# Kernel optimization log

Measured on AMD Instinct MI355X. Metric: run time of the kernel, lower is better.

Reference implementation:

```python
import jax, jax.numpy as jnp
import numpy as np

N, T, I, H = 32, 2048, 256, 512


def setup_inputs() -> dict:
    key = jax.random.key(0)
    k1, k2, k3, k4, k5 = jax.random.split(key, 5)
    x = jax.random.normal(k1, (N, T, I), dtype=jnp.float32)
    initial = jax.random.normal(k2, (N, H), dtype=jnp.float32)
    # nn.Linear default init: U(-1/sqrt(fan_in), 1/sqrt(fan_in))
    s_ih = 1.0 / np.sqrt(I)
    s_hh = 1.0 / np.sqrt(H)
    W_ih = jax.random.uniform(k3, (H, I), jnp.float32, -s_ih, s_ih)
    b_ih = jax.random.uniform(k4, (H,), jnp.float32, -s_ih, s_ih)
    W_hh = jax.random.uniform(k5, (H, H), jnp.float32, -s_hh, s_hh)
    return {"x": x, "initial": initial, "W_ih": W_ih, "b_ih": b_ih, "W_hh": W_hh}


def reference(x, initial, W_ih, b_ih, W_hh):
    # Precompute input projections for all timesteps: [N, T, H]
    proj = jnp.einsum('nti,hi->nth', x, W_ih) + b_ih
    # h_0 = initial + W_ih x_0 + b
    h0 = initial + proj[:, 0]
    # h_t = W_hh h_{t-1} + W_ih x_{t-1} + b  (note: x index is t-1, faithful to source)
    xs = jnp.swapaxes(proj[:, :-1], 0, 1)  # time-major [T-1, N, H], entries t=0..T-2

    def step(h_prev, p):
        h_new = h_prev @ W_hh.T + p
        return h_new, h_new

    _, hs = jax.lax.scan(step, h0, xs)  # [T-1, N, H]
    hiddens = jnp.concatenate([h0[:, None], jnp.swapaxes(hs, 0, 1)], axis=1)  # [N, T, H]
    return (hiddens, hiddens)
```

## Files before the change

kernel.cpp:

```cpp
#include <hip/hip_runtime.h>

#define NB 32
#define TT 2048
#define II 256
#define HH 512
#define LCH 8
#define NCH 256

typedef short s8v __attribute__((ext_vector_type(8)));
typedef short s4v __attribute__((ext_vector_type(4)));
typedef __bf16 bf8v __attribute__((ext_vector_type(8)));
typedef float f4v __attribute__((ext_vector_type(4)));

#define DEVI static __device__ __forceinline__

DEVI float bf2f(short s){ union{unsigned u; float f;} c; c.u = ((unsigned)(unsigned short)s) << 16; return c.f; }
DEVI short f2bf(float f){ union{float f; unsigned u;} c; c.f = f; unsigned u = c.u; u += 0x7FFF + ((u >> 16) & 1); return (short)(u >> 16); }
DEVI f4v fzero(){ f4v z = {0.0f,0.0f,0.0f,0.0f}; return z; }

DEVI f4v mfma16(s8v a, s8v b, f4v c){
  union{ s8v s; bf8v b; } ua, ub; ua.s = a; ub.s = b;
  return __builtin_amdgcn_mfma_f32_16x16x32_bf16(ua.b, ub.b, c, 0, 0, 0);
}

DEVI s8v ldfrag_bf(const short* base, int row0, int ld, int k0, int lane){
  const short* p = base + (size_t)(row0 + (lane & 15)) * ld + k0 + ((lane >> 4) << 3);
  return *(const s8v*)p;
}
DEVI s8v ldfrag_f32(const float* base, int row0, int ld, int k0, int lane){
  const float* p = base + (size_t)(row0 + (lane & 15)) * ld + k0 + ((lane >> 4) << 3);
  f4v lo = *(const f4v*)p;
  f4v hi = *(const f4v*)(p + 4);
  s8v o;
  o[0]=f2bf(lo[0]); o[1]=f2bf(lo[1]); o[2]=f2bf(lo[2]); o[3]=f2bf(lo[3]);
  o[4]=f2bf(hi[0]); o[5]=f2bf(hi[1]); o[6]=f2bf(hi[2]); o[7]=f2bf(hi[3]);
  return o;
}

DEVI int swzoff(int row, int col){ return (row << 9) + ((((col >> 3) ^ (row & 7)) << 3) | (col & 7)); }

#define RAWBAR() asm volatile("s_waitcnt lgkmcnt(0)\n\ts_barrier" ::: "memory")

DEVI void gload16(const void* g, void* l){
  __builtin_amdgcn_global_load_lds((const __attribute__((address_space(1))) void*)g,
                                   (__attribute__((address_space(3))) void*)l, 16, 0, 0);
}

DEVI void stageB(const short* Bt, int ld, int k0, short* btile, int wave, int lane){
  #pragma unroll
  for(int r = 0; r < 8; ++r){
    int slotbase = (((r << 3) + wave) << 6);
    int slot = slotbase + lane;
    int col = slot >> 3, g = slot & 7;
    int gsrc = g ^ (col & 7);
    gload16(Bt + (size_t)col * ld + k0 + (gsrc << 3), btile + ((size_t)slotbase << 3));
  }
}

DEVI s8v ldB(const short* btile, int col, int q, int kk){
  int gphys = ((kk >> 3) + q) ^ (col & 7);
  return *(const s8v*)(btile + (col << 6) + (gphys << 3));
}

__global__ __launch_bounds__(256) void k_init_p1(const float* __restrict__ W,
                                                 short* __restrict__ mats, short* __restrict__ matsT){
  __shared__ short tile[64][65];
  int bx = blockIdx.x, by = blockIdx.y;
  int t = threadIdx.x;
  for(int i = 0; i < 16; ++i){
    int idx = t + 256*i;
    int rr = idx >> 6, cc = idx & 63;
    short v = f2bf(W[(size_t)(64*by + rr)*HH + 64*bx + cc]);
    tile[rr][cc] = v;
    mats[(size_t)(64*by + rr)*HH + 64*bx + cc] = v;
  }
  __syncthreads();
  for(int i = 0; i < 16; ++i){
    int idx = t + 256*i;
    int rr = idx >> 6, cc = idx & 63;
    matsT[(size_t)(64*bx + rr)*HH + 64*by + cc] = tile[cc][rr];
  }
}

__global__ __launch_bounds__(256) void k_cvt(const float* __restrict__ src, short* __restrict__ dst, int n){
  for(int i = blockIdx.x*256 + threadIdx.x; i < n; i += gridDim.x*256) dst[i] = f2bf(src[i]);
}

struct ProdArgs {
  const short* A[8]; const short* Bt[8]; short* C[8]; short* Ct[8];
};
__global__ __launch_bounds__(256) void k_prod(ProdArgs args){
  int bz = blockIdx.z;
  const short* A  = args.A[bz];
  const short* Bt = args.Bt[bz];
  short* C  = args.C[bz];
  short* Ct = args.Ct[bz];
  int wave = threadIdx.x >> 6, lane = threadIdx.x & 63;
  int mrow0 = blockIdx.x*64 + (wave & 1)*32;
  int ncol0 = blockIdx.y*128 + (wave >> 1)*64;
  f4v acc[2][4];
  for(int mi=0;mi<2;mi++) for(int j=0;j<4;j++) acc[mi][j] = fzero();
  for(int k0 = 0; k0 < HH; k0 += 32){
    s8v a0 = ldfrag_bf(A, mrow0,      HH, k0, lane);
    s8v a1 = ldfrag_bf(A, mrow0 + 16, HH, k0, lane);
    #pragma unroll
    for(int j = 0; j < 4; ++j){
      s8v b = ldfrag_bf(Bt, ncol0 + (j<<4), HH, k0, lane);
      acc[0][j] = mfma16(a0, b, acc[0][j]);
      acc[1][j] = mfma16(a1, b, acc[1][j]);
    }
  }
  int q = lane >> 4, c0 = lane & 15;
  for(int mi=0;mi<2;mi++) for(int j=0;j<4;j++) for(int r=0;r<4;r++){
    int row = mrow0 + (mi<<4) + (q<<2) + r;
    int col = ncol0 + (j<<4) + c0;
    short v = f2bf(acc[mi][j][r]);
    C [(size_t)row*HH + col] = v;
    Ct[(size_t)col*HH + row] = v;
  }
}

__global__ __launch_bounds__(512, 4) void k_proj(const float* __restrict__ x, const short* __restrict__ Wb,
                                                 const float* __restrict__ bih, const float* __restrict__ initial,
                                                 short* __restrict__ projb, float* __restrict__ Y00){
  __shared__ __align__(16) short btile[HH*64];
  int b = blockIdx.x;
  int tid = threadIdx.x, wave = tid >> 6, lane = tid & 63;
  int q = lane >> 4, c0 = lane & 15;
  int ncol0 = wave << 6;
  int mrow0 = b << 5;
  f4v acc[2][4];
  #pragma unroll
  for(int mi=0;mi<2;mi++)
  #pragma unroll
  for(int j=0;j<4;j++) acc[mi][j] = fzero();
  s8v a[2][2], an[2][2];
  #pragma unroll
  for(int mi=0;mi<2;++mi)
  #pragma unroll
  for(int k2=0;k2<2;++k2) a[mi][k2] = ldfrag_f32(x, mrow0 + (mi<<4), II, (k2<<5), lane);
  for(int kc = 0; kc < 4; ++kc){
    stageB(Wb, II, kc << 6, btile, wave, lane);
    if(kc < 3){
      #pragma unroll
      for(int mi=0;mi<2;++mi)
      #pragma unroll
      for(int k2=0;k2<2;++k2) an[mi][k2] = ldfrag_f32(x, mrow0 + (mi<<4), II, ((kc+1)<<6)+(k2<<5), lane);
    }
    __syncthreads();
    #pragma unroll
    for(int k2 = 0; k2 < 2; ++k2){
      int kk = k2 << 5;
      #pragma unroll
      for(int j = 0; j < 4; ++j){
        s8v bb = ldB(btile, ncol0 + (j<<4) + c0, q, kk);
        acc[0][j] = mfma16(a[0][k2], bb, acc[0][j]);
        acc[1][j] = mfma16(a[1][k2], bb, acc[1][j]);
      }
    }
    RAWBAR();
    #pragma unroll
    for(int mi=0;mi<2;++mi)
    #pragma unroll
    for(int k2=0;k2<2;++k2) a[mi][k2] = an[mi][k2];
  }
  short* pstage = btile;
  #pragma unroll
  for(int mi=0;mi<2;++mi)
  #pragma unroll
  for(int j=0;j<4;++j)
  #pragma unroll
  for(int r=0;r<4;++r){
    int rown = (mi<<4) + (q<<2) + r;
    int col  = ncol0 + (j<<4) + c0;
    float v = acc[mi][j][r] + bih[col];
    pstage[rown*HH + col] = f2bf(v);
    if(((b & 63) | rown) == 0){
      int n = mrow0 >> 11;
      Y00[(size_t)n*HH + col] = v + initial[(size_t)n*HH + col];
    }
  }
  RAWBAR();
  #pragma unroll
  for(int rr = 0; rr < 4; ++rr){
    int si = tid + (rr << 9);
    int rn = si >> 6, u = (si & 63) << 3;
    *(s8v*)(projb + ((size_t)(mrow0 + rn))*HH + u) = *(const s8v*)(pstage + rn*HH + u);
  }
}

template<int PHASE>
__global__ __launch_bounds__(512, 2) void k_scan(const short* __restrict__ projb,
                                                 const short* __restrict__ Wb,
                                                 const float* __restrict__ Zin,
                                                 float* __restrict__ Yout){
  __shared__ __align__(16) short btile[HH*64];
  __shared__ __align__(16) short st[NB*HH];
  __shared__ __align__(16) short pbuf[NB*HH];
  int c = blockIdx.x;
  int tid = threadIdx.x, wave = tid >> 6, lane = tid & 63;
  int q = lane >> 4, c0 = lane & 15;
  int ncol0 = wave << 6;
  float* fstage = (float*)btile;
  if(PHASE == 0){
    for(int i = tid; i < NB*HH; i += 512) st[i] = 0;
  } else {
    const float* Z = Zin + (size_t)c*NB*HH;
    #pragma unroll
    for(int rr = 0; rr < 8; ++rr){
      int fi = tid + (rr << 9);
      int rn = fi >> 7, col = (fi & 127) << 2;
      f4v v = *(const f4v*)(Z + (size_t)rn*HH + col);
      s4v sv; sv[0]=f2bf(v[0]); sv[1]=f2bf(v[1]); sv[2]=f2bf(v[2]); sv[3]=f2bf(v[3]);
      *(s4v*)(st + swzoff(rn, col)) = sv;
      if(c == 0) *(f4v*)(Yout + ((size_t)rn*TT)*HH + col) = v;
    }
  }
  RAWBAR();
  int tmax = min(LCH, TT - 1 - LCH*c);
  for(int tl = 1; tl <= tmax; ++tl){
    int t = LCH*c + tl;
    #pragma unroll
    for(int r = 0; r < 4; ++r){
      int rn = wave + (r << 3);
      gload16(projb + ((size_t)rn*TT + (t-1))*HH + ((size_t)lane << 3), pbuf + rn*HH);
    }
    f4v acc[2][4];
    #pragma unroll
    for(int mi=0;mi<2;mi++)
    #pragma unroll
    for(int j=0;j<4;j++) acc[mi][j] = fzero();
    for(int kc = 0; kc < 8; ++kc){
      stageB(Wb, HH, kc << 6, btile, wave, lane);
      __syncthreads();
      #pragma unroll
      for(int k2 = 0; k2 < 2; ++k2){
        int kk = k2 << 5;
        int colb = (kc << 6) + kk + (q << 3);
        s8v a0 = *(const s8v*)(st + swzoff(c0,      colb));
        s8v a1 = *(const s8v*)(st + swzoff(c0 + 16, colb));
        #pragma unroll
        for(int j = 0; j < 4; ++j){
          s8v bb = ldB(btile, ncol0 + (j<<4) + c0, q, kk);
          acc[0][j] = mfma16(a0, bb, acc[0][j]);
          acc[1][j] = mfma16(a1, bb, acc[1][j]);
        }
      }
      RAWBAR();
    }
    #pragma unroll
    for(int mi=0;mi<2;++mi)
    #pragma unroll
    for(int j=0;j<4;++j)
    #pragma unroll
    for(int r=0;r<4;++r){
      int rown = (mi<<4) + (q<<2) + r;
      int col  = ncol0 + (j<<4) + c0;
      float v = acc[mi][j][r] + bf2f(pbuf[rown*HH + col]);
      st[swzoff(rown, col)] = f2bf(v);
      if(PHASE == 0){
        if(tl == LCH && c + 1 < NCH)
          Yout[((size_t)(c+1)*NB + rown)*HH + col] = v;
      } else {
        fstage[rown*HH + col] = v;
      }
    }
    if(PHASE == 1){
      RAWBAR();
      #pragma unroll
      for(int rr = 0; rr < 8; ++rr){
        int fi = tid + (rr << 9);
        int rn = fi >> 7, col = (fi & 127) << 2;
        *(f4v*)(Yout + ((size_t)rn*TT + t)*HH + col) = *(const f4v*)(fstage + (size_t)rn*HH + col);
      }
    }
    RAWBAR();
  }
}

__global__ __launch_bounds__(512, 2) void k_ks(const float* __restrict__ Yin, float* __restrict__ Yout,
                                               const short* __restrict__ As, int s){
  __shared__ __align__(16) short btile[HH*64];
  int i = blockIdx.x;
  int tid = threadIdx.x;
  if(i < s){
    const float* src = Yin + (size_t)i*NB*HH;
    float* dst = Yout + (size_t)i*NB*HH;
    for(int fi = tid; fi < NB*HH/4; fi += 512)
      *(f4v*)(dst + ((size_t)fi << 2)) = *(const f4v*)(src + ((size_t)fi << 2));
    return;
  }
  int wave = tid >> 6, lane = tid & 63;
  int q = lane >> 4, c0 = lane & 15;
  int ncol0 = wave << 6;
  const float* Xp = Yin + (size_t)(i - s)*NB*HH;
  const float* Xc = Yin + (size_t)i*NB*HH;
  float* Out = Yout + (size_t)i*NB*HH;
  f4v acc[2][4];
  #pragma unroll
  for(int mi=0;mi<2;mi++)
  #pragma unroll
  for(int j=0;j<4;j++) acc[mi][j] = fzero();
  s8v a[2], an[2];
  a[0] = ldfrag_f32(Xp, 0,  HH, 0, lane);
  a[1] = ldfrag_f32(Xp, 16, HH, 0, lane);
  for(int kc = 0; kc < 8; ++kc){
    stageB(As, HH, kc << 6, btile, wave, lane);
    __syncthreads();
    #pragma unroll
    for(int k2 = 0; k2 < 2; ++k2){
      int kk = k2 << 5;
      int k0n = (kc << 6) + kk + 32;
      if(k0n < HH){
        an[0] = ldfrag_f32(Xp, 0,  HH, k0n, lane);
        an[1] = ldfrag_f32(Xp, 16, HH, k0n, lane);
      }
      #pragma unroll
      for(int j = 0; j < 4; ++j){
        s8v bb = ldB(btile, ncol0 + (j<<4) + c0, q, kk);
        acc[0][j] = mfma16(a[0], bb, acc[0][j]);
        acc[1][j] = mfma16(a[1], bb, acc[1][j]);
      }
      a[0] = an[0]; a[1] = an[1];
    }
    RAWBAR();
  }
  #pragma unroll
  for(int mi=0;mi<2;++mi)
  #pragma unroll
  for(int j=0;j<4;++j)
  #pragma unroll
  for(int r=0;r<4;++r){
    int rown = (mi<<4) + (q<<2) + r;
    int col  = ncol0 + (j<<4) + c0;
    Out[(size_t)rown*HH + col] = acc[mi][j][r] + Xc[(size_t)rown*HH + col];
  }
}

__global__ __launch_bounds__(256) void k_dup(const float* __restrict__ a, float* __restrict__ b, int n4){
  for(int i = blockIdx.x*256 + threadIdx.x; i < n4; i += gridDim.x*256)
    ((f4v*)b)[i] = ((const f4v*)a)[i];
}

extern "C" void kernel_launch(void* const* d_in, const int* in_sizes, int n_in,
                              void* d_out, int out_size, void* d_ws, size_t ws_size,
                              hipStream_t stream) {
  const float* x       = (const float*)d_in[0];
  const float* initial = (const float*)d_in[1];
  const float* Wih     = (const float*)d_in[2];
  const float* bih     = (const float*)d_in[3];
  const float* Whh     = (const float*)d_in[4];
  float* out1 = (float*)d_out;
  float* out2 = out1 + (size_t)NB*TT*HH;
  short* projb = (short*)out2;

  const size_t MSZ = (size_t)HH*HH;
  short* mats  = (short*)d_ws;
  short* matsT = mats + 11*MSZ;
  short* Wihb  = matsT + 11*MSZ;
  float* Y0 = (float*)(Wihb + (size_t)HH*II);
  float* Y1 = out1;

  auto M = [&](int i){ return mats  + (size_t)i*MSZ; };
  auto T = [&](int i){ return matsT + (size_t)i*MSZ; };

  k_init_p1<<<dim3(8,8), 256, 0, stream>>>(Whh, M(0), T(0));
  k_cvt<<<dim3(64), 256, 0, stream>>>(Wih, Wihb, HH*II);

  ProdArgs pa;
  for(int i = 0; i < 10; ++i){
    pa.A[0] = M(i); pa.Bt[0] = T(i); pa.C[0] = M(i+1); pa.Ct[0] = T(i+1);
    k_prod<<<dim3(8,4,1), 256, 0, stream>>>(pa);
  }

  k_proj<<<dim3(2048), 512, 0, stream>>>(x, Wihb, bih, initial, projb, Y0);
  k_scan<0><<<dim3(NCH), 512, 0, stream>>>(projb, M(0), nullptr, Y0);

  float* Ya = Y0; float* Yb = Y1;
  for(int l = 0; l < 8; ++l){
    k_ks<<<dim3(NCH), 512, 0, stream>>>(Ya, Yb, M(3 + l), 1 << l);
    float* tsw = Ya; Ya = Yb; Yb = tsw;
  }

  k_scan<1><<<dim3(NCH), 512, 0, stream>>>(projb, M(0), Y0, out1);
  k_dup<<<dim3(2048), 256, 0, stream>>>(out1, out2, NB*TT*HH/4);
}
```

Baseline: 1.176 ms.

## Store projections in fragment-native layout and drop LDS staging of weights

The input projection kernel now runs one block per timestep and writes its bf16 results in a per-thread fragment layout. The scan kernel can then read each thread's projection values with plain vector loads instead of going through an LDS buffer. The scan and Kogge-Stone kernels read weight fragments straight from global memory (through cache) instead of staging them into LDS with per-chunk barriers. When the workspace is large enough, projections go into the workspace and the final scan writes both output copies directly, removing the separate duplication pass. In exchange, weight traffic now relies on cache hits rather than shared-memory reuse.

```diff
diff --git a/kernel.cpp b/kernel.cpp
--- a/kernel.cpp
+++ b/kernel.cpp
@@ -23,6 +23,13 @@
   return __builtin_amdgcn_mfma_f32_16x16x32_bf16(ua.b, ub.b, c, 0, 0, 0);
 }
 
+DEVI s8v packbf(f4v lo, f4v hi){
+  s8v o;
+  o[0]=f2bf(lo[0]); o[1]=f2bf(lo[1]); o[2]=f2bf(lo[2]); o[3]=f2bf(lo[3]);
+  o[4]=f2bf(hi[0]); o[5]=f2bf(hi[1]); o[6]=f2bf(hi[2]); o[7]=f2bf(hi[3]);
+  return o;
+}
+
 DEVI s8v ldfrag_bf(const short* base, int row0, int ld, int k0, int lane){
   const short* p = base + (size_t)(row0 + (lane & 15)) * ld + k0 + ((lane >> 4) << 3);
   return *(const s8v*)p;
@@ -31,36 +38,18 @@
   const float* p = base + (size_t)(row0 + (lane & 15)) * ld + k0 + ((lane >> 4) << 3);
   f4v lo = *(const f4v*)p;
   f4v hi = *(const f4v*)(p + 4);
-  s8v o;
-  o[0]=f2bf(lo[0]); o[1]=f2bf(lo[1]); o[2]=f2bf(lo[2]); o[3]=f2bf(lo[3]);
-  o[4]=f2bf(hi[0]); o[5]=f2bf(hi[1]); o[6]=f2bf(hi[2]); o[7]=f2bf(hi[3]);
-  return o;
+  return packbf(lo, hi);
+}
+DEVI s8v ldfragX(const float* x, int t, int n0, int k0, int lane){
+  const float* p = x + ((size_t)(n0 + (lane & 15))*TT + t)*II + k0 + ((lane >> 4) << 3);
+  f4v lo = *(const f4v*)p;
+  f4v hi = *(const f4v*)(p + 4);
+  return packbf(lo, hi);
 }
 
 DEVI int swzoff(int row, int col){ return (row << 9) + ((((col >> 3) ^ (row & 7)) << 3) | (col & 7)); }
 
 #define RAWBAR() asm volatile("s_waitcnt lgkmcnt(0)\n\ts_barrier" ::: "memory")
-
-DEVI void gload16(const void* g, void* l){
-  __builtin_amdgcn_global_load_lds((const __attribute__((address_space(1))) void*)g,
-                                   (__attribute__((address_space(3))) void*)l, 16, 0, 0);
-}
-
-DEVI void stageB(const short* Bt, int ld, int k0, short* btile, int wave, int lane){
-  #pragma unroll
-  for(int r = 0; r < 8; ++r){
-    int slotbase = (((r << 3) + wave) << 6);
-    int slot = slotbase + lane;
-    int col = slot >> 3, g = slot & 7;
-    int gsrc = g ^ (col & 7);
-    gload16(Bt + (size_t)col * ld + k0 + (gsrc << 3), btile + ((size_t)slotbase << 3));
-  }
-}
-
-DEVI s8v ldB(const short* btile, int col, int q, int kk){
-  int gphys = ((kk >> 3) + q) ^ (col & 7);
-  return *(const s8v*)(btile + (col << 6) + (gphys << 3));
-}
 
 __global__ __launch_bounds__(256) void k_init_p1(const float* __restrict__ W,
                                                  short* __restrict__ mats, short* __restrict__ matsT){
@@ -120,89 +109,67 @@
   }
 }
 
-__global__ __launch_bounds__(512, 4) void k_proj(const float* __restrict__ x, const short* __restrict__ Wb,
-                                                 const float* __restrict__ bih, const float* __restrict__ initial,
-                                                 short* __restrict__ projb, float* __restrict__ Y00){
-  __shared__ __align__(16) short btile[HH*64];
-  int b = blockIdx.x;
+__global__ __launch_bounds__(512) void k_projT(const float* __restrict__ x, const short* __restrict__ Wb,
+                                               const float* __restrict__ bih, const float* __restrict__ initial,
+                                               short* __restrict__ projF, float* __restrict__ Y00){
+  int t = blockIdx.x;
   int tid = threadIdx.x, wave = tid >> 6, lane = tid & 63;
   int q = lane >> 4, c0 = lane & 15;
   int ncol0 = wave << 6;
-  int mrow0 = b << 5;
   f4v acc[2][4];
   #pragma unroll
   for(int mi=0;mi<2;mi++)
   #pragma unroll
   for(int j=0;j<4;j++) acc[mi][j] = fzero();
-  s8v a[2][2], an[2][2];
+  #pragma unroll
+  for(int kc = 0; kc < 8; ++kc){
+    int k0 = kc << 5;
+    s8v a0 = ldfragX(x, t, 0,  k0, lane);
+    s8v a1 = ldfragX(x, t, 16, k0, lane);
+    #pragma unroll
+    for(int j = 0; j < 4; ++j){
+      s8v bb = ldfrag_bf(Wb, ncol0 + (j<<4), II, k0, lane);
+      acc[0][j] = mfma16(a0, bb, acc[0][j]);
+      acc[1][j] = mfma16(a1, bb, acc[1][j]);
+    }
+  }
+  float bv[4];
+  #pragma unroll
+  for(int j=0;j<4;++j) bv[j] = bih[ncol0 + (j<<4) + c0];
+  s8v pv[4];
   #pragma unroll
   for(int mi=0;mi<2;++mi)
   #pragma unroll
-  for(int k2=0;k2<2;++k2) a[mi][k2] = ldfrag_f32(x, mrow0 + (mi<<4), II, (k2<<5), lane);
-  for(int kc = 0; kc < 4; ++kc){
-    stageB(Wb, II, kc << 6, btile, wave, lane);
-    if(kc < 3){
-      #pragma unroll
-      for(int mi=0;mi<2;++mi)
-      #pragma unroll
-      for(int k2=0;k2<2;++k2) an[mi][k2] = ldfrag_f32(x, mrow0 + (mi<<4), II, ((kc+1)<<6)+(k2<<5), lane);
-    }
-    __syncthreads();
-    #pragma unroll
-    for(int k2 = 0; k2 < 2; ++k2){
-      int kk = k2 << 5;
-      #pragma unroll
-      for(int j = 0; j < 4; ++j){
-        s8v bb = ldB(btile, ncol0 + (j<<4) + c0, q, kk);
-        acc[0][j] = mfma16(a[0][k2], bb, acc[0][j]);
-        acc[1][j] = mfma16(a[1][k2], bb, acc[1][j]);
-      }
-    }
-    RAWBAR();
-    #pragma unroll
-    for(int mi=0;mi<2;++mi)
-    #pragma unroll
-    for(int k2=0;k2<2;++k2) a[mi][k2] = an[mi][k2];
-  }
-  short* pstage = btile;
-  #pragma unroll
-  for(int mi=0;mi<2;++mi)
-  #pragma unroll
   for(int j=0;j<4;++j)
   #pragma unroll
   for(int r=0;r<4;++r){
-    int rown = (mi<<4) + (q<<2) + r;
-    int col  = ncol0 + (j<<4) + c0;
-    float v = acc[mi][j][r] + bih[col];
-    pstage[rown*HH + col] = f2bf(v);
-    if(((b & 63) | rown) == 0){
-      int n = mrow0 >> 11;
+    int idx = (mi<<4) | (j<<2) | r;
+    float v = acc[mi][j][r] + bv[j];
+    pv[idx>>3][idx&7] = f2bf(v);
+    if(t == 0){
+      int n = (mi<<4) + (q<<2) + r;
+      int col = ncol0 + (j<<4) + c0;
       Y00[(size_t)n*HH + col] = v + initial[(size_t)n*HH + col];
     }
   }
-  RAWBAR();
-  #pragma unroll
-  for(int rr = 0; rr < 4; ++rr){
-    int si = tid + (rr << 9);
-    int rn = si >> 6, u = (si & 63) << 3;
-    *(s8v*)(projb + ((size_t)(mrow0 + rn))*HH + u) = *(const s8v*)(pstage + rn*HH + u);
-  }
-}
-
-template<int PHASE>
-__global__ __launch_bounds__(512, 2) void k_scan(const short* __restrict__ projb,
-                                                 const short* __restrict__ Wb,
-                                                 const float* __restrict__ Zin,
-                                                 float* __restrict__ Yout){
-  __shared__ __align__(16) short btile[HH*64];
+  short* dst = projF + (((size_t)t << 9) + tid)*32;
+  #pragma unroll
+  for(int g = 0; g < 4; ++g) *(s8v*)(dst + (g<<3)) = pv[g];
+}
+
+template<int PHASE, int DUAL>
+__global__ __launch_bounds__(512) void k_scan(const short* __restrict__ projF,
+                                              const short* __restrict__ Wb,
+                                              const float* __restrict__ Zin,
+                                              float* __restrict__ Yout,
+                                              float* __restrict__ Yout2){
   __shared__ __align__(16) short st[NB*HH];
-  __shared__ __align__(16) short pbuf[NB*HH];
+  __shared__ __align__(16) float fstage[PHASE==1 ? NB*HH : 4];
   int c = blockIdx.x;
   int tid = threadIdx.x, wave = tid >> 6, lane = tid & 63;
   int q = lane >> 4, c0 = lane & 15;
   int ncol0 = wave << 6;
-  float* fstage = (float*)btile;
-  if(PHASE == 0){
+  if constexpr(PHASE == 0){
     for(int i = tid; i < NB*HH; i += 512) st[i] = 0;
   } else {
     const float* Z = Zin + (size_t)c*NB*HH;
@@ -213,74 +180,78 @@
       f4v v = *(const f4v*)(Z + (size_t)rn*HH + col);
       s4v sv; sv[0]=f2bf(v[0]); sv[1]=f2bf(v[1]); sv[2]=f2bf(v[2]); sv[3]=f2bf(v[3]);
       *(s4v*)(st + swzoff(rn, col)) = sv;
-      if(c == 0) *(f4v*)(Yout + ((size_t)rn*TT)*HH + col) = v;
+      if(c == 0){
+        *(f4v*)(Yout + ((size_t)rn*TT)*HH + col) = v;
+        if(DUAL) *(f4v*)(Yout2 + ((size_t)rn*TT)*HH + col) = v;
+      }
     }
   }
   RAWBAR();
   int tmax = min(LCH, TT - 1 - LCH*c);
   for(int tl = 1; tl <= tmax; ++tl){
     int t = LCH*c + tl;
-    #pragma unroll
-    for(int r = 0; r < 4; ++r){
-      int rn = wave + (r << 3);
-      gload16(projb + ((size_t)rn*TT + (t-1))*HH + ((size_t)lane << 3), pbuf + rn*HH);
-    }
+    const short* pb = projF + (((size_t)(t-1) << 9) + tid)*32;
+    s8v pp[4];
+    pp[0] = *(const s8v*)(pb);
+    pp[1] = *(const s8v*)(pb + 8);
+    pp[2] = *(const s8v*)(pb + 16);
+    pp[3] = *(const s8v*)(pb + 24);
     f4v acc[2][4];
     #pragma unroll
     for(int mi=0;mi<2;mi++)
     #pragma unroll
     for(int j=0;j<4;j++) acc[mi][j] = fzero();
-    for(int kc = 0; kc < 8; ++kc){
-      stageB(Wb, HH, kc << 6, btile, wave, lane);
-      __syncthreads();
+    #pragma unroll
+    for(int kc = 0; kc < 16; ++kc){
+      int k0 = kc << 5;
+      int colb = k0 + (q << 3);
+      s8v a0 = *(const s8v*)(st + swzoff(c0,      colb));
+      s8v a1 = *(const s8v*)(st + swzoff(c0 + 16, colb));
       #pragma unroll
-      for(int k2 = 0; k2 < 2; ++k2){
-        int kk = k2 << 5;
-        int colb = (kc << 6) + kk + (q << 3);
-        s8v a0 = *(const s8v*)(st + swzoff(c0,      colb));
-        s8v a1 = *(const s8v*)(st + swzoff(c0 + 16, colb));
-        #pragma unroll
-        for(int j = 0; j < 4; ++j){
-          s8v bb = ldB(btile, ncol0 + (j<<4) + c0, q, kk);
-          acc[0][j] = mfma16(a0, bb, acc[0][j]);
-          acc[1][j] = mfma16(a1, bb, acc[1][j]);
-        }
+      for(int j = 0; j < 4; ++j){
+        s8v bb = ldfrag_bf(Wb, ncol0 + (j<<4), HH, k0, lane);
+        acc[0][j] = mfma16(a0, bb, acc[0][j]);
+        acc[1][j] = mfma16(a1, bb, acc[1][j]);
       }
-      RAWBAR();
-    }
+    }
+    RAWBAR();
     #pragma unroll
     for(int mi=0;mi<2;++mi)
     #pragma unroll
     for(int j=0;j<4;++j)
     #pragma unroll
     for(int r=0;r<4;++r){
+      int idx = (mi<<4) | (j<<2) | r;
       int rown = (mi<<4) + (q<<2) + r;
       int col  = ncol0 + (j<<4) + c0;
-      float v = acc[mi][j][r] + bf2f(pbuf[rown*HH + col]);
+      float v = acc[mi][j][r] + bf2f(pp[idx>>3][idx&7]);
       st[swzoff(rown, col)] = f2bf(v);
-      if(PHASE == 0){
+      if constexpr(PHASE == 0){
         if(tl == LCH && c + 1 < NCH)
           Yout[((size_t)(c+1)*NB + rown)*HH + col] = v;
       } else {
         fstage[rown*HH + col] = v;
       }
     }
-    if(PHASE == 1){
+    if constexpr(PHASE == 1){
       RAWBAR();
       #pragma unroll
       for(int rr = 0; rr < 8; ++rr){
         int fi = tid + (rr << 9);
         int rn = fi >> 7, col = (fi & 127) << 2;
-        *(f4v*)(Yout + ((size_t)rn*TT + t)*HH + col) = *(const f4v*)(fstage + (size_t)rn*HH + col);
+        f4v v = *(const f4v*)(fstage + (size_t)rn*HH + col);
+        *(f4v*)(Yout + ((size_t)rn*TT + t)*HH + col) = v;
+        if(DUAL) *(f4v*)(Yout2 + ((size_t)rn*TT + t)*HH + col) = v;
       }
-    }
-    RAWBAR();
-  }
-}
-
-__global__ __launch_bounds__(512, 2) void k_ks(const float* __restrict__ Yin, float* __restrict__ Yout,
-                                               const short* __restrict__ As, int s){
-  __shared__ __align__(16) short btile[HH*64];
+    } else {
+      RAWBAR();
+    }
+  }
+}
+
+__global__ __launch_bounds__(512) void k_ks(const float* __restrict__ Yin, float* __restrict__ Yout,
+                                            const short* __restrict__ As, int s){
+  __shared__ __align__(16) float fstage[NB*HH];
   int i = blockIdx.x;
   int tid = threadIdx.x;
   if(i < s){
@@ -301,29 +272,17 @@
   for(int mi=0;mi<2;mi++)
   #pragma unroll
   for(int j=0;j<4;j++) acc[mi][j] = fzero();
-  s8v a[2], an[2];
-  a[0] = ldfrag_f32(Xp, 0,  HH, 0, lane);
-  a[1] = ldfrag_f32(Xp, 16, HH, 0, lane);
-  for(int kc = 0; kc < 8; ++kc){
-    stageB(As, HH, kc << 6, btile, wave, lane);
-    __syncthreads();
-    #pragma unroll
-    for(int k2 = 0; k2 < 2; ++k2){
-      int kk = k2 << 5;
-      int k0n = (kc << 6) + kk + 32;
-      if(k0n < HH){
-        an[0] = ldfrag_f32(Xp, 0,  HH, k0n, lane);
-        an[1] = ldfrag_f32(Xp, 16, HH, k0n, lane);
-      }
-      #pragma unroll
-      for(int j = 0; j < 4; ++j){
-        s8v bb = ldB(btile, ncol0 + (j<<4) + c0, q, kk);
-        acc[0][j] = mfma16(a[0], bb, acc[0][j]);
-        acc[1][j] = mfma16(a[1], bb, acc[1][j]);
-      }
-      a[0] = an[0]; a[1] = an[1];
-    }
-    RAWBAR();
+  #pragma unroll
+  for(int kc = 0; kc < 16; ++kc){
+    int k0 = kc << 5;
+    s8v a0 = ldfrag_f32(Xp, 0,  HH, k0, lane);
+    s8v a1 = ldfrag_f32(Xp, 16, HH, k0, lane);
+    #pragma unroll
+    for(int j = 0; j < 4; ++j){
+      s8v bb = ldfrag_bf(As, ncol0 + (j<<4), HH, k0, lane);
+      acc[0][j] = mfma16(a0, bb, acc[0][j]);
+      acc[1][j] = mfma16(a1, bb, acc[1][j]);
+    }
   }
   #pragma unroll
   for(int mi=0;mi<2;++mi)
@@ -333,7 +292,17 @@
   for(int r=0;r<4;++r){
     int rown = (mi<<4) + (q<<2) + r;
     int col  = ncol0 + (j<<4) + c0;
-    Out[(size_t)rown*HH + col] = acc[mi][j][r] + Xc[(size_t)rown*HH + col];
+    fstage[(size_t)rown*HH + col] = acc[mi][j][r];
+  }
+  RAWBAR();
+  #pragma unroll
+  for(int rr = 0; rr < 8; ++rr){
+    int fi = tid + (rr << 9);
+    int rn = fi >> 7, col = (fi & 127) << 2;
+    f4v v = *(const f4v*)(fstage + (size_t)rn*HH + col);
+    f4v xc = *(const f4v*)(Xc + (size_t)rn*HH + col);
+    v = v + xc;
+    *(f4v*)(Out + (size_t)rn*HH + col) = v;
   }
 }
 
@@ -352,7 +321,6 @@
   const float* Whh     = (const float*)d_in[4];
   float* out1 = (float*)d_out;
   float* out2 = out1 + (size_t)NB*TT*HH;
-  short* projb = (short*)out2;
 
   const size_t MSZ = (size_t)HH*HH;
   short* mats  = (short*)d_ws;
@@ -360,6 +328,10 @@
   short* Wihb  = matsT + 11*MSZ;
   float* Y0 = (float*)(Wihb + (size_t)HH*II);
   float* Y1 = out1;
+  short* projw = (short*)(Y0 + (size_t)NCH*NB*HH);
+  size_t need = (size_t)((char*)(projw + (size_t)NB*TT*HH) - (char*)d_ws);
+  bool dual = ws_size >= need;
+  short* projF = dual ? projw : (short*)out2;
 
   auto M = [&](int i){ return mats  + (size_t)i*MSZ; };
   auto T = [&](int i){ return matsT + (size_t)i*MSZ; };
@@ -373,8 +345,8 @@
     k_prod<<<dim3(8,4,1), 256, 0, stream>>>(pa);
   }
 
-  k_proj<<<dim3(2048), 512, 0, stream>>>(x, Wihb, bih, initial, projb, Y0);
-  k_scan<0><<<dim3(NCH), 512, 0, stream>>>(projb, M(0), nullptr, Y0);
+  k_projT<<<dim3(TT), 512, 0, stream>>>(x, Wihb, bih, initial, projF, Y0);
+  k_scan<0,0><<<dim3(NCH), 512, 0, stream>>>(projF, M(0), nullptr, Y0, nullptr);
 
   float* Ya = Y0; float* Yb = Y1;
   for(int l = 0; l < 8; ++l){
@@ -382,6 +354,10 @@
     float* tsw = Ya; Ya = Yb; Yb = tsw;
   }
 
-  k_scan<1><<<dim3(NCH), 512, 0, stream>>>(projb, M(0), Y0, out1);
-  k_dup<<<dim3(2048), 256, 0, stream>>>(out1, out2, NB*TT*HH/4);
-}
+  if(dual){
+    k_scan<1,1><<<dim3(NCH), 512, 0, stream>>>(projF, M(0), Y0, out1, out2);
+  } else {
+    k_scan<1,0><<<dim3(NCH), 512, 0, stream>>>(projF, M(0), Y0, out1, out1);
+    k_dup<<<dim3(2048), 256, 0, stream>>>(out1, out2, NB*TT*HH/4);
+  }
+}
```

Result: slower. 1.296 ms (+10.2%).
